# Optimization experiments

Hardware: AMD Instinct MI355X
Metric: run time of the kernel (lower is better)

The kernel has to match this reference:

```python
import jax, jax.numpy as jnp
import numpy as np

# Model dims (match init_kwargs / module defaults)
B, D, H, E, K, DEPTH, BS = 8192, 1024, 4096, 16, 2, 2, 64
SP_EXPERT, SP_CROSS = 0.85, 0.9  # block sparsities


def _block_mask(key, n_in, n_out, sparsity):
    """Bool mask [n_in, n_out] with (BS x BS)-block structure, ~(1-sparsity) dense.
    Matches torch.rand(n_blocks_out, n_blocks_in) > sparsity, expanded to full size."""
    mb = jax.random.uniform(key, (n_out // BS, n_in // BS)) > sparsity  # [ob, ib]
    return jnp.repeat(jnp.repeat(mb.T, BS, axis=0), BS, axis=1)  # [n_in, n_out]


def setup_inputs() -> dict:
    key = jax.random.key(0)
    ks = jax.random.split(key, 12)
    x = jax.random.normal(ks[0], (B, D), dtype=jnp.float32)
    gate_w = jax.random.normal(ks[1], (DEPTH, E, D), dtype=jnp.float32) / np.sqrt(D)
    temperature = jnp.ones((DEPTH,), dtype=jnp.float32)
    w1 = jax.random.normal(ks[2], (E, D, H), dtype=jnp.float32) * 0.02
    b1 = jnp.zeros((E, H), dtype=jnp.float32)
    w2 = jax.random.normal(ks[3], (E, H, D), dtype=jnp.float32) * 0.02
    b2 = jnp.zeros((E, D), dtype=jnp.float32)
    cross_w = jax.random.normal(ks[4], (D, D), dtype=jnp.float32) * 0.02
    cross_b = jnp.zeros((D,), dtype=jnp.float32)
    mk = jax.random.split(ks[5], 2 * E + 1)
    mask1 = jnp.stack([_block_mask(mk[i], D, H, SP_EXPERT) for i in range(E)])
    mask2 = jnp.stack([_block_mask(mk[E + i], H, D, SP_EXPERT) for i in range(E)])
    cross_mask = _block_mask(mk[2 * E], D, D, SP_CROSS)
    return {"x": x, "gate_w": gate_w, "temperature": temperature,
            "w1": w1, "b1": b1, "w2": w2, "b2": b2,
            "cross_w": cross_w, "cross_b": cross_b,
            "mask1": mask1, "mask2": mask2, "cross_mask": cross_mask}


def reference(x, gate_w, temperature, w1, b1, w2, b2, cross_w, cross_b,
              mask1, mask2, cross_mask):
    n_tok = x.shape[0]
    # Only the last-depth router affects the output (x is never updated and
    # expert_outputs is re-initialized each depth iteration in the original).
    logits = jnp.einsum('bd,ed->be', x, gate_w[-1]) / temperature[-1]
    top_vals, top_idx = jax.lax.top_k(logits, K)            # [n_tok, K]
    rout_w = jax.nn.softmax(top_vals, axis=-1)
    routing = jnp.zeros((n_tok, E), x.dtype).at[
        jnp.arange(n_tok)[:, None], top_idx].set(rout_w)    # [n_tok, E]

    expert_out = jnp.zeros_like(x)
    for e in range(E):  # fixed small expert count
        h = jax.nn.silu(x @ (w1[e] * mask1[e]) + b1[e])     # [n_tok, H]
        y = h @ (w2[e] * mask2[e]) + b2[e]                  # [n_tok, D]
        expert_out = expert_out + y * routing[:, e:e + 1]
    return x + expert_out @ (cross_w * cross_mask) + cross_b
```

## Files before the change

### kernel.cpp

```cpp
#include <hip/hip_runtime.h>


#define NTOK 8192
#define DIM  1024
#define HID  4096
#define NEXP 16
#define BM   256
#define ROWS_CAP (NTOK*2 + NEXP*256)

typedef __attribute__((ext_vector_type(4))) float fx4;
typedef __attribute__((ext_vector_type(4))) unsigned int ux4;
typedef __attribute__((ext_vector_type(2))) unsigned int ux2;
typedef __attribute__((ext_vector_type(8))) short s8v;
union V16 { ux4 u; s8v s; };

__device__ __forceinline__ unsigned int f2bf(float f) {
  unsigned int u = __float_as_uint(f);
  return (u + 0x7fffu + ((u >> 16) & 1u)) >> 16;
}

__device__ __forceinline__ unsigned int cvt_pk(float lo, float hi) {
  unsigned int r;
  asm("v_cvt_pk_bf16_f32 %0, %1, %2" : "=v"(r) : "v"(lo), "v"(hi));
  return r;
}

__device__ __forceinline__ unsigned int f2fp8(float v) {
  return (unsigned int)__builtin_amdgcn_cvt_pk_fp8_f32(v, v, 0, false) & 0xFFu;
}

__device__ __forceinline__ unsigned int pk4fp8(float a, float b, float c, float d) {
  unsigned int u = (unsigned int)__builtin_amdgcn_cvt_pk_fp8_f32(a, b, 0, false);
  u = (unsigned int)__builtin_amdgcn_cvt_pk_fp8_f32(c, d, (int)u, true);
  return u;
}

__device__ __forceinline__ bool mask_at(const void* m, int flag, size_t idx) {
  if (flag == 0) return ((const unsigned char*)m)[idx] != 0;
  if (flag == 1) return ((const int*)m)[idx] != 0;
  return ((const float*)m)[idx] != 0.0f;
}

__device__ __forceinline__ int flag_of(int ev) {
  return (ev & 2) ? 2 : ((ev & 1) ? 0 : 1);
}

__device__ __forceinline__ int xcd_swz() {
  const int b = blockIdx.x, cpx = gridDim.x >> 3;
  return (b & 7) * cpx + (b >> 3);
}

__global__ void k_route(const float* __restrict__ x,
                        const float* __restrict__ gw,
                        const float* __restrict__ temp,
                        const unsigned int* __restrict__ m1raw,
                        int* __restrict__ top2i, float* __restrict__ top2w,
                        int* __restrict__ meta, unsigned char* __restrict__ x8)
{
  if (blockIdx.x < 64) {
    int bits = 0;
    size_t base = (size_t)blockIdx.x * 4096 + threadIdx.x;
    for (int j = 0; j < 16; j++) {
      unsigned int v = m1raw[base + 256 * j];
      if (v == 0x3f800000u) bits |= 2;
      else if (v > 1u)      bits |= 1;
    }
    if (bits) atomicOr(&meta[1], bits);
  }

  __shared__ float gwsh[NEXP * DIM];
  for (int i = threadIdx.x; i < NEXP * DIM; i += 256) gwsh[i] = gw[i];
  __syncthreads();

  const int wv = threadIdx.x >> 6;
  const int l = threadIdx.x & 63;
  #pragma unroll
  for (int tt = 0; tt < 8; tt++) {
    const int t = blockIdx.x * 32 + wv * 8 + tt;
    const float* xr = x + (size_t)t * DIM;
    float xv[16];
    #pragma unroll
    for (int j = 0; j < 16; j++) xv[j] = xr[l + 64 * j];
    float logit[16];
    #pragma unroll
    for (int e = 0; e < 16; e++) {
      const float* g = gwsh + e * DIM;
      float s = 0.f;
      #pragma unroll
      for (int j = 0; j < 16; j++) s += xv[j] * g[l + 64 * j];
      #pragma unroll
      for (int o = 32; o >= 1; o >>= 1) s += __shfl_xor(s, o);
      logit[e] = s;
    }
    if (l == 0) {
      const float tinv = 1.0f / temp[0];
      int i0 = 0; float v0 = logit[0] * tinv;
      #pragma unroll
      for (int e = 1; e < 16; e++) { float v = logit[e] * tinv; if (v > v0) { v0 = v; i0 = e; } }
      int i1 = -1; float v1 = 0.f; bool first = true;
      #pragma unroll
      for (int e = 0; e < 16; e++) {
        if (e == i0) continue;
        float v = logit[e] * tinv;
        if (first || v > v1) { v1 = v; i1 = e; first = false; }
      }
      float ex = __expf(v1 - v0);
      float den = 1.0f + ex;
      top2i[2 * t] = i0; top2i[2 * t + 1] = i1;
      top2w[2 * t] = 1.0f / den; top2w[2 * t + 1] = ex / den;
      atomicAdd(&meta[8 + i0], 1);
      atomicAdd(&meta[8 + i1], 1);
    }
  }

  {
    const size_t be = (size_t)blockIdx.x * 32 * DIM;
    const fx4* src = (const fx4*)(x + be);
    ux4* dst = (ux4*)(x8 + be);
    #pragma unroll
    for (int i = 0; i < 8; i++) {
      const int idx = i * 256 + threadIdx.x;
      fx4 a = src[4 * idx], b = src[4 * idx + 1];
      fx4 c = src[4 * idx + 2], d = src[4 * idx + 3];
      ux4 o;
      o[0] = pk4fp8(a[0] * 16.f, a[1] * 16.f, a[2] * 16.f, a[3] * 16.f);
      o[1] = pk4fp8(b[0] * 16.f, b[1] * 16.f, b[2] * 16.f, b[3] * 16.f);
      o[2] = pk4fp8(c[0] * 16.f, c[1] * 16.f, c[2] * 16.f, c[3] * 16.f);
      o[3] = pk4fp8(d[0] * 16.f, d[1] * 16.f, d[2] * 16.f, d[3] * 16.f);
      dst[idx] = o;
    }
  }
}

__global__ void k_offsets(int* __restrict__ meta, int* __restrict__ tok_of_row) {
  if (threadIdx.x == 0) {
    int o = 0;
    for (int e = 0; e < 16; e++) { meta[32 + e] = o; o += (meta[8 + e] + 255) & ~255; }
    meta[48] = o;
    for (int rt = 0; rt < ROWS_CAP / BM; rt++) {
      const int base = rt * BM;
      int e = 0;
      for (int i = 1; i < 16; i++) if (meta[32 + i] <= base) e = i;
      meta[96 + rt] = e;
    }
  }
  __syncthreads();
  const int total = meta[48];
  for (int r = threadIdx.x; r < total; r += 256) {
    const int e = meta[96 + r / BM];
    if (r >= meta[32 + e] + meta[8 + e]) tok_of_row[r] = -1;
  }
}

__global__ void k_assign(const int* __restrict__ top2i,
                         const float* __restrict__ top2w,
                         int* __restrict__ meta, int* __restrict__ tok_of_row,
                         int* __restrict__ t2row)
{
  int t = blockIdx.x * 256 + threadIdx.x;
  if (t >= NTOK) return;
  #pragma unroll
  for (int k = 0; k < 2; k++) {
    int e = top2i[2 * t + k];
    int slot = atomicAdd(&meta[64 + e], 1);
    int row = meta[32 + e] + slot;
    tok_of_row[row] = t;
    t2row[2 * t + k] = row;
  }
}

__global__ __launch_bounds__(256, 4)
void k_gemm1(const unsigned char* __restrict__ x8,
             const float* __restrict__ w1, const float* __restrict__ b1,
             const void* __restrict__ mask1,
             const int* __restrict__ meta, const int* __restrict__ tok_of_row,
             unsigned char* __restrict__ h8)
{
  __shared__ ux4 Ash[2][1024];
  __shared__ __align__(16) unsigned int Bsh[2][1024];

  const int bid = xcd_swz();
  const int rt = bid >> 6, ct = bid & 63;
  const int base = rt * BM;
  if (base >= meta[48]) return;
  const int e = meta[96 + rt];

  const int tid = threadIdx.x;
  const int wv = tid >> 6;
  const int jg0 = ct * 64;
  const int l = tid & 63, l16 = l & 15, lhi = l >> 4;

  unsigned int bits;
  {
    const int flag = flag_of(meta[1]);
    bool on = false;
    if (l < 16)
      on = mask_at(mask1, flag, (size_t)e * DIM * HID + (size_t)l * 64 * HID + jg0);
    bits = (unsigned int)(__ballot(on) & 0xFFFFull);
  }

  const unsigned int sw = (unsigned int)((tid & 3) ^ ((tid >> 3) & 3));
  unsigned int aoff[4];
  #pragma unroll
  for (int i = 0; i < 4; i++) {
    int tok = tok_of_row[base + i * 64 + (tid >> 2)];
    if (tok < 0) tok = 0;
    aoff[i] = (unsigned int)tok * (unsigned int)DIM + sw * 16;
  }

  const int kb = tid >> 4, jb = tid & 15;

  fx4 acc[4][4] = {};

  auto STAGE_A = [&](int b, int d0) {
    const char* gp = (const char*)x8 + d0;
    #pragma unroll
    for (int i = 0; i < 4; i++)
      __builtin_amdgcn_global_load_lds(
        (const __attribute__((address_space(1))) unsigned int*)(gp + aoff[i]),
        (__attribute__((address_space(3))) unsigned int*)&Ash[b][i * 256 + wv * 64],
        16, 0, 0);
  };
  auto LOAD_B = [&](fx4* r, int d0) {
    const float* bp = w1 + ((size_t)e * DIM + d0 + kb * 4) * HID + jg0 + jb * 4;
    r[0] = *(const fx4*)bp;
    r[1] = *(const fx4*)(bp + HID);
    r[2] = *(const fx4*)(bp + 2 * HID);
    r[3] = *(const fx4*)(bp + 3 * HID);
  };
  auto WRITE_B = [&](int b, const fx4* r) {
    #pragma unroll
    for (int jj = 0; jj < 4; jj++) {
      const int col = jb * 4 + jj;
      unsigned int u = pk4fp8(r[0][jj] * 16.0f, r[1][jj] * 16.0f,
                              r[2][jj] * 16.0f, r[3][jj] * 16.0f);
      Bsh[b][col * 16 + (((kb >> 2) ^ ((col >> 1) & 3)) << 2) + (kb & 3)] = u;
    }
  };
  auto COMPUTE = [&](int b) {
    const char* Ab = (const char*)&Ash[b][0];
    const char* Bb = (const char*)&Bsh[b][0];
    #pragma unroll
    for (int ks = 0; ks < 2; ks++) {
      const int c = ks * 2 + (lhi >> 1);
      const int sub = (lhi & 1) << 3;
      long long a[4], bb[4];
      #pragma unroll
      for (int m = 0; m < 4; m++) {
        const int row = wv * 64 + m * 16 + l16;
        a[m] = *(const long long*)(Ab + row * 64 + ((c ^ ((row >> 1) & 3)) << 4) + sub);
      }
      #pragma unroll
      for (int n = 0; n < 4; n++) {
        const int col = n * 16 + l16;
        bb[n] = *(const long long*)(Bb + col * 64 + ((c ^ ((col >> 1) & 3)) << 4) + sub);
      }
      #pragma unroll
      for (int m = 0; m < 4; m++)
        #pragma unroll
        for (int n = 0; n < 4; n++)
          acc[m][n] = __builtin_amdgcn_mfma_f32_16x16x32_fp8_fp8(a[m], bb[n], acc[m][n], 0, 0, 0);
    }
  };

  if (bits) {
    int d0 = (__ffs(bits) - 1) << 6; bits &= bits - 1;
    {
      fx4 br[4];
      STAGE_A(0, d0);
      LOAD_B(br, d0);
      WRITE_B(0, br);
    }
    __syncthreads();
    int cur = 0;
    for (;;) {
      int nd0 = -1;
      fx4 br2[4];
      if (bits) { nd0 = (__ffs(bits) - 1) << 6; bits &= bits - 1; }
      if (nd0 >= 0) { STAGE_A(cur ^ 1, nd0); LOAD_B(br2, nd0); }
      COMPUTE(cur);
      if (nd0 >= 0) WRITE_B(cur ^ 1, br2);
      __syncthreads();
      cur ^= 1;
      if (nd0 < 0) break;
    }
  }

  unsigned char* hs = (unsigned char*)&Ash[0][0];
  __syncthreads();
  #pragma unroll
  for (int m = 0; m < 4; m++)
    #pragma unroll
    for (int n = 0; n < 4; n++) {
      const int gcol = jg0 + n * 16 + l16;
      const float bbv = b1[e * HID + gcol];
      #pragma unroll
      for (int i = 0; i < 4; i++) {
        const int row = wv * 64 + m * 16 + lhi * 4 + i;
        float v = acc[m][n][i] * 0.00390625f + bbv;
        float hval = v / (1.0f + __expf(-v));
        hs[row * 64 + n * 16 + l16] = (unsigned char)f2fp8(hval * 8.0f);
      }
    }
  __syncthreads();
  {
    const ux4* s = (const ux4*)hs;
    #pragma unroll
    for (int j = 0; j < 4; j++) {
      const int c2 = j * 256 + tid;
      const int row = c2 >> 2;
      *(ux4*)(h8 + (size_t)(base + row) * HID + ct * 64 + (c2 & 3) * 16) = s[c2];
    }
  }
}

__global__ __launch_bounds__(256, 4)
void k_gemm2(const unsigned char* __restrict__ h8,
             const float* __restrict__ w2, const float* __restrict__ b2,
             const void* __restrict__ mask2,
             const int* __restrict__ meta, unsigned short* __restrict__ yb)
{
  __shared__ ux4 Ash[2][1024];
  __shared__ __align__(16) unsigned int Bsh[2][1024];

  const int bid = xcd_swz();
  const int rt = bid >> 4, ct = bid & 15;
  const int base = rt * BM;
  if (base >= meta[48]) return;
  const int e = meta[96 + rt];

  const int tid = threadIdx.x;
  const int wv = tid >> 6;
  const int jg0 = ct * 64;

  const int l = tid & 63, l16 = l & 15, lhi = l >> 4;
  unsigned long long bits;
  {
    const int flag = flag_of(meta[1]);
    bits = __ballot(mask_at(mask2, flag,
             (size_t)e * HID * DIM + (size_t)l * 64 * DIM + jg0));
  }

  const unsigned int sw = (unsigned int)((tid & 3) ^ ((tid >> 3) & 3));
  unsigned int aoff[4];
  #pragma unroll
  for (int i = 0; i < 4; i++)
    aoff[i] = (unsigned int)(base + i * 64 + (tid >> 2)) * (unsigned int)HID + sw * 16;

  const int kb = tid >> 4, jb = tid & 15;

  fx4 acc[4][4] = {};

  auto STAGE_A = [&](int b, int d0) {
    const char* gp = (const char*)h8 + d0;
    #pragma unroll
    for (int i = 0; i < 4; i++)
      __builtin_amdgcn_global_load_lds(
        (const __attribute__((address_space(1))) unsigned int*)(gp + aoff[i]),
        (__attribute__((address_space(3))) unsigned int*)&Ash[b][i * 256 + wv * 64],
        16, 0, 0);
  };
  auto LOAD_B = [&](fx4* r, int d0) {
    const float* bp = w2 + ((size_t)e * HID + d0 + kb * 4) * DIM + jg0 + jb * 4;
    r[0] = *(const fx4*)bp;
    r[1] = *(const fx4*)(bp + DIM);
    r[2] = *(const fx4*)(bp + 2 * DIM);
    r[3] = *(const fx4*)(bp + 3 * DIM);
  };
  auto WRITE_B = [&](int b, const fx4* r) {
    #pragma unroll
    for (int jj = 0; jj < 4; jj++) {
      const int col = jb * 4 + jj;
      unsigned int u = pk4fp8(r[0][jj] * 16.0f, r[1][jj] * 16.0f,
                              r[2][jj] * 16.0f, r[3][jj] * 16.0f);
      Bsh[b][col * 16 + (((kb >> 2) ^ ((col >> 1) & 3)) << 2) + (kb & 3)] = u;
    }
  };
  auto COMPUTE = [&](int b) {
    const char* Ab = (const char*)&Ash[b][0];
    const char* Bb = (const char*)&Bsh[b][0];
    #pragma unroll
    for (int ks = 0; ks < 2; ks++) {
      const int c = ks * 2 + (lhi >> 1);
      const int sub = (lhi & 1) << 3;
      long long a[4], bb[4];
      #pragma unroll
      for (int m = 0; m < 4; m++) {
        const int row = wv * 64 + m * 16 + l16;
        a[m] = *(const long long*)(Ab + row * 64 + ((c ^ ((row >> 1) & 3)) << 4) + sub);
      }
      #pragma unroll
      for (int n = 0; n < 4; n++) {
        const int col = n * 16 + l16;
        bb[n] = *(const long long*)(Bb + col * 64 + ((c ^ ((col >> 1) & 3)) << 4) + sub);
      }
      #pragma unroll
      for (int m = 0; m < 4; m++)
        #pragma unroll
        for (int n = 0; n < 4; n++)
          acc[m][n] = __builtin_amdgcn_mfma_f32_16x16x32_fp8_fp8(a[m], bb[n], acc[m][n], 0, 0, 0);
    }
  };

  if (bits) {
    int d0 = (__ffsll(bits) - 1) << 6; bits &= bits - 1;
    {
      fx4 br[4];
      STAGE_A(0, d0);
      LOAD_B(br, d0);
      WRITE_B(0, br);
    }
    __syncthreads();
    int cur = 0;
    for (;;) {
      int nd0 = -1;
      fx4 br2[4];
      if (bits) { nd0 = (__ffsll(bits) - 1) << 6; bits &= bits - 1; }
      if (nd0 >= 0) { STAGE_A(cur ^ 1, nd0); LOAD_B(br2, nd0); }
      COMPUTE(cur);
      if (nd0 >= 0) WRITE_B(cur ^ 1, br2);
      __syncthreads();
      cur ^= 1;
      if (nd0 < 0) break;
    }
  }

  unsigned short* hs = (unsigned short*)&Ash[0][0];
  __syncthreads();
  #pragma unroll
  for (int m = 0; m < 4; m++)
    #pragma unroll
    for (int n = 0; n < 4; n++) {
      const int gcol = jg0 + n * 16 + l16;
      const float bbv = b2[e * DIM + gcol];
      #pragma unroll
      for (int i = 0; i < 4; i++) {
        const int row = wv * 64 + m * 16 + lhi * 4 + i;
        hs[row * 64 + n * 16 + l16] =
            (unsigned short)f2bf(acc[m][n][i] * 0.0078125f + bbv);
      }
    }
  __syncthreads();
  {
    const ux4* s = (const ux4*)hs;
    #pragma unroll
    for (int j = 0; j < 8; j++) {
      const int c2 = j * 256 + tid;
      const int row = c2 >> 3;
      *(ux4*)(yb + (size_t)(base + row) * DIM + ct * 64 + (c2 & 7) * 8) = s[c2];
    }
  }
}

__global__ __launch_bounds__(256, 4)
void k_cross(const unsigned short* __restrict__ yb, const float* __restrict__ x,
             const float* __restrict__ cw, const float* __restrict__ cb,
             const void* __restrict__ cmask, const int* __restrict__ meta,
             const int* __restrict__ t2row, const float* __restrict__ t2w,
             float* __restrict__ out)
{
  __shared__ ux4 Ash[1024];
  __shared__ __align__(16) ux2 Bsh[1024];

  const int bid = xcd_swz();
  const int rt = bid >> 4, ct = bid & 15;
  const int base = rt * 128;
  const int tid = threadIdx.x;
  const int wv = tid >> 6;
  const int wr = wv >> 1, wc = wv & 1;
  const int jg0 = ct * 64;

  const int l = tid & 63, l16 = l & 15, lhi = l >> 4;

  unsigned int bits;
  {
    const int flag = flag_of(meta[1]);
    bool on = false;
    if (l < 16)
      on = mask_at(cmask, flag, (size_t)l * 64 * DIM + jg0);
    bits = (unsigned int)(__ballot(on) & 0xFFFFull);
  }

  const int arow = tid >> 1, sub = tid & 1;
  const int r0 = t2row[2 * (base + arow)], r1 = t2row[2 * (base + arow) + 1];
  const float w0 = t2w[2 * (base + arow)], w1 = t2w[2 * (base + arow) + 1];

  fx4 acc[4][2] = {};

  while (bits) {
    const int kbx = __ffs(bits) - 1; bits &= bits - 1;
    const int d0 = kbx * 64;
    {
      const ux4* s0 = (const ux4*)(yb + (size_t)r0 * DIM + d0);
      const ux4* s1 = (const ux4*)(yb + (size_t)r1 * DIM + d0);
      #pragma unroll
      for (int s = 0; s < 4; s++) {
        const int seg = sub * 4 + s;
        ux4 v0 = s0[seg], v1 = s1[seg], o;
        #pragma unroll
        for (int j = 0; j < 4; j++) {
          float alo = __uint_as_float(v0[j] << 16);
          float ahi = __uint_as_float(v0[j] & 0xFFFF0000u);
          float blo = __uint_as_float(v1[j] << 16);
          float bhi = __uint_as_float(v1[j] & 0xFFFF0000u);
          o[j] = cvt_pk(w0 * alo + w1 * blo, w0 * ahi + w1 * bhi);
        }
        Ash[arow * 8 + (seg ^ (arow & 7))] = o;
      }
    }
    {
      const int kbt = tid >> 4, jb = tid & 15;
      const float* bp = cw + (size_t)(d0 + kbt * 4) * DIM + jg0 + jb * 4;
      fx4 r0v = *(const fx4*)bp;
      fx4 r1v = *(const fx4*)(bp + DIM);
      fx4 r2v = *(const fx4*)(bp + 2 * DIM);
      fx4 r3v = *(const fx4*)(bp + 3 * DIM);
      #pragma unroll
      for (int jj = 0; jj < 4; jj++) {
        ux2 val;
        val[0] = cvt_pk(r0v[jj], r1v[jj]);
        val[1] = cvt_pk(r2v[jj], r3v[jj]);
        const int col = jb * 4 + jj;
        Bsh[(col * 8 + ((kbt >> 1) ^ (col & 7))) * 2 + (kbt & 1)] = val;
      }
    }
    __syncthreads();
    #pragma unroll
    for (int ks = 0; ks < 2; ks++) {
      s8v a[4], b[2];
      const int seg = ks * 4 + lhi;
      #pragma unroll
      for (int m = 0; m < 4; m++) {
        const int row = wr * 64 + m * 16 + l16;
        V16 v; v.u = Ash[row * 8 + (seg ^ (row & 7))]; a[m] = v.s;
      }
      #pragma unroll
      for (int n = 0; n < 2; n++) {
        const int col = wc * 32 + n * 16 + l16;
        V16 v; v.u = ((const ux4*)Bsh)[col * 8 + (seg ^ (col & 7))]; b[n] = v.s;
      }
      #pragma unroll
      for (int m = 0; m < 4; m++)
        #pragma unroll
        for (int n = 0; n < 2; n++)
          acc[m][n] = __builtin_amdgcn_mfma_f32_16x16x32_bf16(a[m], b[n], acc[m][n], 0, 0, 0);
    }
    __syncthreads();
  }

  #pragma unroll
  for (int m = 0; m < 4; m++)
    #pragma unroll
    for (int n = 0; n < 2; n++) {
      const int gcol = jg0 + wc * 32 + n * 16 + l16;
      #pragma unroll
      for (int i = 0; i < 4; i++) {
        const int row = wr * 64 + m * 16 + lhi * 4 + i;
        const size_t idx = (size_t)(base + row) * DIM + gcol;
        out[idx] = acc[m][n][i] + x[idx] + cb[gcol];
      }
    }
}

extern "C" void kernel_launch(void* const* d_in, const int* in_sizes, int n_in,
                              void* d_out, int out_size, void* d_ws, size_t ws_size,
                              hipStream_t stream)
{
  (void)in_sizes; (void)n_in; (void)out_size; (void)ws_size;
  const float* x      = (const float*)d_in[0];
  const float* gate_w = (const float*)d_in[1];
  const float* temp   = (const float*)d_in[2];
  const float* w1     = (const float*)d_in[3];
  const float* b1     = (const float*)d_in[4];
  const float* w2     = (const float*)d_in[5];
  const float* b2     = (const float*)d_in[6];
  const float* cw     = (const float*)d_in[7];
  const float* cb     = (const float*)d_in[8];
  const void*  mask1  = d_in[9];
  const void*  mask2  = d_in[10];
  const void*  cmask  = d_in[11];
  float* out = (float*)d_out;
  char* ws = (char*)d_ws;

  size_t off = 0;
  auto walloc = [&](size_t b) { size_t r = off; off = (off + b + 255) & ~(size_t)255; return r; };
  size_t o_meta = walloc(4096);
  size_t o_t2i  = walloc((size_t)NTOK * 2 * 4);
  size_t o_t2w  = walloc((size_t)NTOK * 2 * 4);
  size_t o_t2r  = walloc((size_t)NTOK * 2 * 4);
  size_t o_tok  = walloc((size_t)ROWS_CAP * 4);
  size_t o_x8   = walloc((size_t)NTOK * DIM);
  size_t o_y    = walloc((size_t)ROWS_CAP * DIM * 2);
  size_t o_hc   = walloc((size_t)ROWS_CAP * HID);

  int*                meta = (int*)(ws + o_meta);
  int*                t2i  = (int*)(ws + o_t2i);
  float*              t2w  = (float*)(ws + o_t2w);
  int*                t2r  = (int*)(ws + o_t2r);
  int*                tok  = (int*)(ws + o_tok);
  unsigned char*      x8   = (unsigned char*)(ws + o_x8);
  unsigned short*     yb   = (unsigned short*)(ws + o_y);
  unsigned char*      h8   = (unsigned char*)(ws + o_hc);

  hipMemsetAsync(ws + o_meta, 0, 4096, stream);

  k_route  <<<NTOK / 32, 256, 0, stream>>>(x, gate_w + (size_t)1 * NEXP * DIM, temp + 1,
                                           (const unsigned int*)mask1, t2i, t2w, meta, x8);
  k_offsets<<<1, 256, 0, stream>>>(meta, tok);
  k_assign <<<NTOK / 256, 256, 0, stream>>>(t2i, t2w, meta, tok, t2r);

  const int NRT = ROWS_CAP / BM;
  k_gemm1<<<NRT * 64, 256, 0, stream>>>(x8, w1, b1, mask1, meta, tok, h8);
  k_gemm2<<<NRT * 16, 256, 0, stream>>>(h8, w2, b2, mask2, meta, yb);
  k_cross<<<(NTOK / 128) * 16, 256, 0, stream>>>(yb, x, cw, cb, cmask, meta, t2r, t2w, out);
}
```

Before: 345.8 us.

## Pre-cast masked expert weights to swizzled fp8 tiles before the GEMMs

Adds a k_wcast kernel that converts only the nonzero 64x64 weight blocks of w1 and w2 to fp8, once per call, into a pre-swizzled tile layout in workspace. The two GEMMs then stage B directly into LDS with global_load_lds instead of loading fp32 and converting in registers. Previously each row tile re-read and re-converted the same fp32 weights, so this is meant to cut redundant fp32 traffic and conversion work inside the GEMM loops. The cost is an extra launch, an fp8 weight buffer in workspace and a one-time full read of the active weight blocks.

```diff
diff --git a/kernel.cpp b/kernel.cpp
--- a/kernel.cpp
+++ b/kernel.cpp
@@ -132,6 +132,46 @@
   }
 }
 
+__global__ void k_wcast(const float* __restrict__ w1, const float* __restrict__ w2,
+                        const void* __restrict__ mask1, const void* __restrict__ mask2,
+                        const int* __restrict__ meta,
+                        unsigned char* __restrict__ w1p, unsigned char* __restrict__ w2p)
+{
+  const int flag = flag_of(meta[1]);
+  const int gid = blockIdx.x;
+  const int tid = threadIdx.x;
+  const int c = tid >> 6, col = tid & 63;
+
+  if (gid < 16384) {
+    const int p = gid >> 4, kb = gid & 15;
+    const int e = p >> 6, ct = p & 63;
+    if (!mask_at(mask1, flag, (size_t)e * DIM * HID + (size_t)kb * 64 * HID + ct * 64)) return;
+    const float* src = w1 + ((size_t)e * DIM + kb * 64 + c * 16) * HID + ct * 64 + col;
+    ux4 v;
+    #pragma unroll
+    for (int q = 0; q < 4; q++) {
+      float f0 = src[(size_t)(q * 4 + 0) * HID], f1 = src[(size_t)(q * 4 + 1) * HID];
+      float f2 = src[(size_t)(q * 4 + 2) * HID], f3 = src[(size_t)(q * 4 + 3) * HID];
+      v[q] = pk4fp8(f0 * 16.f, f1 * 16.f, f2 * 16.f, f3 * 16.f);
+    }
+    *(ux4*)(w1p + ((size_t)gid << 12) + col * 64 + ((c ^ ((col >> 1) & 3)) << 4)) = v;
+  } else {
+    const int g2 = gid - 16384;
+    const int p = g2 >> 6, kb = g2 & 63;
+    const int e = p >> 4, ct = p & 15;
+    if (!mask_at(mask2, flag, (size_t)e * HID * DIM + (size_t)kb * 64 * DIM + ct * 64)) return;
+    const float* src = w2 + ((size_t)e * HID + kb * 64 + c * 16) * DIM + ct * 64 + col;
+    ux4 v;
+    #pragma unroll
+    for (int q = 0; q < 4; q++) {
+      float f0 = src[(size_t)(q * 4 + 0) * DIM], f1 = src[(size_t)(q * 4 + 1) * DIM];
+      float f2 = src[(size_t)(q * 4 + 2) * DIM], f3 = src[(size_t)(q * 4 + 3) * DIM];
+      v[q] = pk4fp8(f0 * 16.f, f1 * 16.f, f2 * 16.f, f3 * 16.f);
+    }
+    *(ux4*)(w2p + ((size_t)g2 << 12) + col * 64 + ((c ^ ((col >> 1) & 3)) << 4)) = v;
+  }
+}
+
 __global__ void k_offsets(int* __restrict__ meta, int* __restrict__ tok_of_row) {
   if (threadIdx.x == 0) {
     int o = 0;
@@ -171,7 +211,7 @@
 
 __global__ __launch_bounds__(256, 4)
 void k_gemm1(const unsigned char* __restrict__ x8,
-             const float* __restrict__ w1, const float* __restrict__ b1,
+             const unsigned char* __restrict__ w1p, const float* __restrict__ b1,
              const void* __restrict__ mask1,
              const int* __restrict__ meta, const int* __restrict__ tok_of_row,
              unsigned char* __restrict__ h8)
@@ -208,8 +248,6 @@
     aoff[i] = (unsigned int)tok * (unsigned int)DIM + sw * 16;
   }
 
-  const int kb = tid >> 4, jb = tid & 15;
-
   fx4 acc[4][4] = {};
 
   auto STAGE_A = [&](int b, int d0) {
@@ -221,21 +259,12 @@
         (__attribute__((address_space(3))) unsigned int*)&Ash[b][i * 256 + wv * 64],
         16, 0, 0);
   };
-  auto LOAD_B = [&](fx4* r, int d0) {
-    const float* bp = w1 + ((size_t)e * DIM + d0 + kb * 4) * HID + jg0 + jb * 4;
-    r[0] = *(const fx4*)bp;
-    r[1] = *(const fx4*)(bp + HID);
-    r[2] = *(const fx4*)(bp + 2 * HID);
-    r[3] = *(const fx4*)(bp + 3 * HID);
-  };
-  auto WRITE_B = [&](int b, const fx4* r) {
-    #pragma unroll
-    for (int jj = 0; jj < 4; jj++) {
-      const int col = jb * 4 + jj;
-      unsigned int u = pk4fp8(r[0][jj] * 16.0f, r[1][jj] * 16.0f,
-                              r[2][jj] * 16.0f, r[3][jj] * 16.0f);
-      Bsh[b][col * 16 + (((kb >> 2) ^ ((col >> 1) & 3)) << 2) + (kb & 3)] = u;
-    }
+  auto STAGE_B = [&](int b, int kb) {
+    const char* src = (const char*)w1p + (((size_t)(e * 64 + ct) * 16 + kb) << 12) + tid * 16;
+    __builtin_amdgcn_global_load_lds(
+      (const __attribute__((address_space(1))) unsigned int*)src,
+      (__attribute__((address_space(3))) unsigned int*)&Bsh[b][wv * 256],
+      16, 0, 0);
   };
   auto COMPUTE = [&](int b) {
     const char* Ab = (const char*)&Ash[b][0];
@@ -264,25 +293,18 @@
   };
 
   if (bits) {
-    int d0 = (__ffs(bits) - 1) << 6; bits &= bits - 1;
-    {
-      fx4 br[4];
-      STAGE_A(0, d0);
-      LOAD_B(br, d0);
-      WRITE_B(0, br);
-    }
+    int kb0 = __ffs(bits) - 1; bits &= bits - 1;
+    STAGE_A(0, kb0 << 6); STAGE_B(0, kb0);
     __syncthreads();
     int cur = 0;
     for (;;) {
-      int nd0 = -1;
-      fx4 br2[4];
-      if (bits) { nd0 = (__ffs(bits) - 1) << 6; bits &= bits - 1; }
-      if (nd0 >= 0) { STAGE_A(cur ^ 1, nd0); LOAD_B(br2, nd0); }
+      int nkb = -1;
+      if (bits) { nkb = __ffs(bits) - 1; bits &= bits - 1; }
+      if (nkb >= 0) { STAGE_A(cur ^ 1, nkb << 6); STAGE_B(cur ^ 1, nkb); }
       COMPUTE(cur);
-      if (nd0 >= 0) WRITE_B(cur ^ 1, br2);
       __syncthreads();
       cur ^= 1;
-      if (nd0 < 0) break;
+      if (nkb < 0) break;
     }
   }
 
@@ -316,7 +338,7 @@
 
 __global__ __launch_bounds__(256, 4)
 void k_gemm2(const unsigned char* __restrict__ h8,
-             const float* __restrict__ w2, const float* __restrict__ b2,
+             const unsigned char* __restrict__ w2p, const float* __restrict__ b2,
              const void* __restrict__ mask2,
              const int* __restrict__ meta, unsigned short* __restrict__ yb)
 {
@@ -347,8 +369,6 @@
   for (int i = 0; i < 4; i++)
     aoff[i] = (unsigned int)(base + i * 64 + (tid >> 2)) * (unsigned int)HID + sw * 16;
 
-  const int kb = tid >> 4, jb = tid & 15;
-
   fx4 acc[4][4] = {};
 
   auto STAGE_A = [&](int b, int d0) {
@@ -360,21 +380,12 @@
         (__attribute__((address_space(3))) unsigned int*)&Ash[b][i * 256 + wv * 64],
         16, 0, 0);
   };
-  auto LOAD_B = [&](fx4* r, int d0) {
-    const float* bp = w2 + ((size_t)e * HID + d0 + kb * 4) * DIM + jg0 + jb * 4;
-    r[0] = *(const fx4*)bp;
-    r[1] = *(const fx4*)(bp + DIM);
-    r[2] = *(const fx4*)(bp + 2 * DIM);
-    r[3] = *(const fx4*)(bp + 3 * DIM);
-  };
-  auto WRITE_B = [&](int b, const fx4* r) {
-    #pragma unroll
-    for (int jj = 0; jj < 4; jj++) {
-      const int col = jb * 4 + jj;
-      unsigned int u = pk4fp8(r[0][jj] * 16.0f, r[1][jj] * 16.0f,
-                              r[2][jj] * 16.0f, r[3][jj] * 16.0f);
-      Bsh[b][col * 16 + (((kb >> 2) ^ ((col >> 1) & 3)) << 2) + (kb & 3)] = u;
-    }
+  auto STAGE_B = [&](int b, int kb) {
+    const char* src = (const char*)w2p + (((size_t)(e * 16 + ct) * 64 + kb) << 12) + tid * 16;
+    __builtin_amdgcn_global_load_lds(
+      (const __attribute__((address_space(1))) unsigned int*)src,
+      (__attribute__((address_space(3))) unsigned int*)&Bsh[b][wv * 256],
+      16, 0, 0);
   };
   auto COMPUTE = [&](int b) {
     const char* Ab = (const char*)&Ash[b][0];
@@ -403,25 +414,18 @@
   };
 
   if (bits) {
-    int d0 = (__ffsll(bits) - 1) << 6; bits &= bits - 1;
-    {
-      fx4 br[4];
-      STAGE_A(0, d0);
-      LOAD_B(br, d0);
-      WRITE_B(0, br);
-    }
+    int kb0 = __ffsll(bits) - 1; bits &= bits - 1;
+    STAGE_A(0, kb0 << 6); STAGE_B(0, kb0);
     __syncthreads();
     int cur = 0;
     for (;;) {
-      int nd0 = -1;
-      fx4 br2[4];
-      if (bits) { nd0 = (__ffsll(bits) - 1) << 6; bits &= bits - 1; }
-      if (nd0 >= 0) { STAGE_A(cur ^ 1, nd0); LOAD_B(br2, nd0); }
+      int nkb = -1;
+      if (bits) { nkb = __ffsll(bits) - 1; bits &= bits - 1; }
+      if (nkb >= 0) { STAGE_A(cur ^ 1, nkb << 6); STAGE_B(cur ^ 1, nkb); }
       COMPUTE(cur);
-      if (nd0 >= 0) WRITE_B(cur ^ 1, br2);
       __syncthreads();
       cur ^= 1;
-      if (nd0 < 0) break;
+      if (nkb < 0) break;
     }
   }
 
@@ -592,6 +596,8 @@
   size_t o_x8   = walloc((size_t)NTOK * DIM);
   size_t o_y    = walloc((size_t)ROWS_CAP * DIM * 2);
   size_t o_hc   = walloc((size_t)ROWS_CAP * HID);
+  size_t o_w1p  = walloc((size_t)16384 * 4096);
+  size_t o_w2p  = walloc((size_t)16384 * 4096);
 
   int*                meta = (int*)(ws + o_meta);
   int*                t2i  = (int*)(ws + o_t2i);
@@ -601,16 +607,19 @@
   unsigned char*      x8   = (unsigned char*)(ws + o_x8);
   unsigned short*     yb   = (unsigned short*)(ws + o_y);
   unsigned char*      h8   = (unsigned char*)(ws + o_hc);
+  unsigned char*      w1p  = (unsigned char*)(ws + o_w1p);
+  unsigned char*      w2p  = (unsigned char*)(ws + o_w2p);
 
   hipMemsetAsync(ws + o_meta, 0, 4096, stream);
 
   k_route  <<<NTOK / 32, 256, 0, stream>>>(x, gate_w + (size_t)1 * NEXP * DIM, temp + 1,
                                            (const unsigned int*)mask1, t2i, t2w, meta, x8);
+  k_wcast  <<<32768, 256, 0, stream>>>(w1, w2, mask1, mask2, meta, w1p, w2p);
   k_offsets<<<1, 256, 0, stream>>>(meta, tok);
   k_assign <<<NTOK / 256, 256, 0, stream>>>(t2i, t2w, meta, tok, t2r);
 
   const int NRT = ROWS_CAP / BM;
-  k_gemm1<<<NRT * 64, 256, 0, stream>>>(x8, w1, b1, mask1, meta, tok, h8);
-  k_gemm2<<<NRT * 16, 256, 0, stream>>>(h8, w2, b2, mask2, meta, yb);
+  k_gemm1<<<NRT * 64, 256, 0, stream>>>(x8, w1p, b1, mask1, meta, tok, h8);
+  k_gemm2<<<NRT * 16, 256, 0, stream>>>(h8, w2p, b2, mask2, meta, yb);
   k_cross<<<(NTOK / 128) * 16, 256, 0, stream>>>(yb, x, cw, cb, cmask, meta, t2r, t2w, out);
 }
```

Result: faster. 336.4 us (-2.7%).
